# Optimization experiments

Hardware: AMD Instinct MI355X
Metric: run time of the kernel (lower is better)

Reference implementation:

```python
import jax, jax.numpy as jnp
import numpy as np

B, S, D = 1, 2048, 2048
NH, NKV = 32, 8
HD = D // NH  # 64
ROPE_THETA = 10000.0


def setup_inputs() -> dict:
    key = jax.random.key(0)
    k1, k2, k3 = jax.random.split(key, 3)
    x = jax.random.normal(k1, (B, S, D), dtype=jnp.float32)
    # real RoPE frequencies (freqs_cis = exp(i * t * theta^(-2j/hd)))
    inv_freq = 1.0 / (ROPE_THETA ** (np.arange(0, HD, 2, dtype=np.float32) / HD))
    t = np.arange(S, dtype=np.float32)
    ang = np.outer(t, inv_freq)  # [S, HD/2]
    cos = jnp.asarray(np.cos(ang), dtype=jnp.float32)
    sin = jnp.asarray(np.sin(ang), dtype=jnp.float32)
    wqkv = jax.random.normal(k2, (NH * HD + 2 * NKV * HD, D), dtype=jnp.float32) * (D ** -0.5)
    wo = jax.random.normal(k3, (D, NH * HD), dtype=jnp.float32) * (D ** -0.5)
    return {"x": x, "cos": cos, "sin": sin, "wqkv": wqkv, "wo": wo}


def _rope(t, cos, sin):
    # t: [b, h, s, hd]; pairs are interleaved (even=real, odd=imag)
    tr = t[..., 0::2]
    ti = t[..., 1::2]
    c = cos[None, None]  # [1,1,s,hd/2]
    s_ = sin[None, None]
    orr = tr * c - ti * s_
    oi = tr * s_ + ti * c
    out = jnp.stack([orr, oi], axis=-1)  # [b,h,s,hd/2,2]
    return out.reshape(t.shape)


def reference(x, cos, sin, wqkv, wo):
    bsz, seqlen, d_model = x.shape
    qkv = jnp.einsum('bsd,ed->bse', x, wqkv)  # fused QKV proj
    q, k, v = jnp.split(qkv, [NH * HD, NH * HD + NKV * HD], axis=-1)
    q = q.reshape(bsz, seqlen, NH, HD).transpose(0, 2, 1, 3)
    k = k.reshape(bsz, seqlen, NKV, HD).transpose(0, 2, 1, 3)
    v = v.reshape(bsz, seqlen, NKV, HD).transpose(0, 2, 1, 3)
    q = _rope(q, cos, sin)
    k = _rope(k, cos, sin)
    # GQA: repeat_interleave kv heads
    rep = NH // NKV
    k_r = jnp.broadcast_to(k[:, :, None], (bsz, NKV, rep, seqlen, HD)).reshape(bsz, NH, seqlen, HD)
    v_r = jnp.broadcast_to(v[:, :, None], (bsz, NKV, rep, seqlen, HD)).reshape(bsz, NH, seqlen, HD)
    scale = 1.0 / jnp.sqrt(jnp.asarray(HD, dtype=x.dtype))
    scores = jnp.einsum('bhqd,bhkd->bhqk', q, k_r) * scale
    causal = jnp.tril(jnp.ones((seqlen, seqlen), dtype=bool))
    scores = jnp.where(causal[None, None], scores, jnp.asarray(-jnp.inf, dtype=scores.dtype))
    attn = jax.nn.softmax(scores, axis=-1)
    y = jnp.einsum('bhqk,bhkd->bhqd', attn, v_r)
    y = y.transpose(0, 2, 1, 3).reshape(bsz, seqlen, NH * HD)
    y = jnp.einsum('bse,de->bsd', y, wo)
    return y
```

## Files before the change

kernel.cpp:

```cpp
#include <hip/hip_runtime.h>
#include <hip/hip_bf16.h>

typedef __attribute__((ext_vector_type(8))) short bf16x8;
typedef __attribute__((ext_vector_type(4))) float f32x4;
typedef __attribute__((ext_vector_type(16))) float f32x16;
typedef __attribute__((ext_vector_type(2))) unsigned int u32x2;

#define S_LEN 2048
#define DMODEL 2048
#define NHEAD 32
#define NKVH 8
#define HDIM 64
#define EQKV 3072

#if defined(__has_builtin)
#if __has_builtin(__builtin_amdgcn_global_load_lds)
#define HAVE_GLL 1
#endif
#endif

__device__ __forceinline__ unsigned short f2bf(float f) {
  unsigned int u = __float_as_uint(f);
  u = (u + 0x7FFFu + ((u >> 16) & 1u)) >> 16;
  return (unsigned short)u;
}

__device__ __forceinline__ f32x4 mfma16(bf16x8 a, bf16x8 b, f32x4 c) {
  return __builtin_amdgcn_mfma_f32_16x16x32_bf16(a, b, c, 0, 0, 0);
}
__device__ __forceinline__ f32x16 mfma32(bf16x8 a, bf16x8 b, f32x16 c) {
  return __builtin_amdgcn_mfma_f32_32x32x16_bf16(a, b, c, 0, 0, 0);
}

__device__ __forceinline__ unsigned cvtpk(float a, float b) {
  unsigned r;
  asm("v_cvt_pk_bf16_f32 %0, %1, %2" : "=v"(r) : "v"(a), "v"(b));
  return r;
}

__device__ __forceinline__ void plswap(unsigned& a, unsigned& b) {
  u32x2 r = __builtin_amdgcn_permlane32_swap(a, b, false, false);
  a = r.x;
  b = r.y;
}
__device__ __forceinline__ void plswapf(float& a, float& b) {
  unsigned ua = __float_as_uint(a), ub = __float_as_uint(b);
  plswap(ua, ub);
  a = __uint_as_float(ua);
  b = __uint_as_float(ub);
}

#if HAVE_GLL
__device__ __forceinline__ void gload16(const unsigned short* g,
                                        unsigned short* l) {
  __builtin_amdgcn_global_load_lds(
      (const __attribute__((address_space(1))) unsigned int*)g,
      (__attribute__((address_space(3))) unsigned int*)l, 16, 0, 0);
}
#endif

__global__ void cast_kernel(const float* __restrict__ src,
                            unsigned short* __restrict__ dst, int n4) {
  int i = blockIdx.x * blockDim.x + threadIdx.x;
  if (i >= n4) return;
  float4 v = ((const float4*)src)[i];
  ushort4 o;
  o.x = f2bf(v.x); o.y = f2bf(v.y); o.z = f2bf(v.z); o.w = f2bf(v.w);
  ((ushort4*)dst)[i] = o;
}

__launch_bounds__(256)
__global__ void gemm_bt(const unsigned short* __restrict__ A,
                        const unsigned short* __restrict__ B,
                        float* __restrict__ C, int M, int N, int K) {
  __shared__ unsigned short As[128 * 64];
  __shared__ unsigned short Bs[128 * 64];
  const int tid = threadIdx.x;
  const int w = tid >> 6, l = tid & 63;
  const int wr = w >> 1, wc = w & 1;
  const int bm = blockIdx.y, bn = blockIdx.x;
  const int lr = l & 15, lq = l >> 4;

  f32x4 acc[4][4];
#pragma unroll
  for (int m = 0; m < 4; ++m)
#pragma unroll
    for (int n = 0; n < 4; ++n) acc[m][n] = (f32x4)0.f;

  const unsigned short* gA[4];
  const unsigned short* gB[4];
#pragma unroll
  for (int i = 0; i < 4; ++i) {
    int c = i * 256 + tid;
    int row = c >> 3;
    int sc = (c & 7) ^ (row & 7);
    gA[i] = A + (size_t)(bm * 128 + row) * K + sc * 8;
    gB[i] = B + (size_t)(bn * 128 + row) * K + sc * 8;
  }

  for (int k0 = 0; k0 < K; k0 += 64) {
#if HAVE_GLL
#pragma unroll
    for (int i = 0; i < 4; ++i) {
      gload16(gA[i] + k0, &As[(i * 256 + w * 64) * 8]);
      gload16(gB[i] + k0, &Bs[(i * 256 + w * 64) * 8]);
    }
#else
#pragma unroll
    for (int i = 0; i < 4; ++i) {
      int c = i * 256 + tid;
      *(uint4*)(&As[c * 8]) = *(const uint4*)(gA[i] + k0);
      *(uint4*)(&Bs[c * 8]) = *(const uint4*)(gB[i] + k0);
    }
#endif
    __syncthreads();
#pragma unroll
    for (int ks = 0; ks < 2; ++ks) {
      bf16x8 af[4], bfr[4];
#pragma unroll
      for (int m = 0; m < 4; ++m) {
        int row = wr * 64 + m * 16 + lr;
        int ch = (ks * 4 + lq) ^ (row & 7);
        af[m] = *(const bf16x8*)(&As[row * 64 + ch * 8]);
      }
#pragma unroll
      for (int n = 0; n < 4; ++n) {
        int row = wc * 64 + n * 16 + lr;
        int ch = (ks * 4 + lq) ^ (row & 7);
        bfr[n] = *(const bf16x8*)(&Bs[row * 64 + ch * 8]);
      }
#pragma unroll
      for (int m = 0; m < 4; ++m)
#pragma unroll
        for (int n = 0; n < 4; ++n)
          acc[m][n] = mfma16(af[m], bfr[n], acc[m][n]);
    }
    __syncthreads();
  }
  const int r0 = bm * 128 + wr * 64;
  const int c0 = bn * 128 + wc * 64;
#pragma unroll
  for (int m = 0; m < 4; ++m)
#pragma unroll
    for (int n = 0; n < 4; ++n)
#pragma unroll
      for (int r = 0; r < 4; ++r)
        C[(size_t)(r0 + m * 16 + 4 * lq + r) * N + c0 + n * 16 + lr] =
            acc[m][n][r];
}

#define KSCALE 0.18033688011112042f
__global__ void rope_split(const float* __restrict__ qkv,
                           const float* __restrict__ cosb,
                           const float* __restrict__ sinb,
                           unsigned short* __restrict__ qb,
                           unsigned short* __restrict__ kft) {
  const int s = blockIdx.x;
  const float* row = qkv + (size_t)s * EQKV;
  for (int idx = threadIdx.x; idx < 1280; idx += 256) {
    int hh = idx >> 5;
    int m = idx & 31;
    float c = cosb[s * 32 + m];
    float sn = sinb[s * 32 + m];
    if (hh < 32) {
      float tr = row[hh * 64 + 2 * m];
      float ti = row[hh * 64 + 2 * m + 1];
      unsigned int pack = (unsigned int)f2bf(tr * c - ti * sn) |
                          ((unsigned int)f2bf(tr * sn + ti * c) << 16);
      *(unsigned int*)(qb + ((size_t)hh * S_LEN + s) * HDIM + 2 * m) = pack;
    } else {
      int kvh = hh - 32;
      float cs = c * KSCALE, ss = sn * KSCALE;
      float tr = row[2048 + kvh * 64 + 2 * m];
      float ti = row[2048 + kvh * 64 + 2 * m + 1];
      unsigned int pack = (unsigned int)f2bf(tr * cs - ti * ss) |
                          ((unsigned int)f2bf(tr * ss + ti * cs) << 16);
      int kt = s >> 5, lq = s & 31;
      int j = m >> 3, hi = (m >> 2) & 1;
      unsigned short* dst =
          kft +
          ((((size_t)kvh * 64 + kt) * 4 + j) * 64 + lq + 32 * hi) * 8 +
          (m & 3) * 2;
      *(unsigned int*)dst = pack;
    }
  }
}

__global__ void v_transpose(const float* __restrict__ qkv,
                            unsigned short* __restrict__ vft) {
  __shared__ unsigned short tile[64][72];
  const int kvh = blockIdx.x;
  const int st = blockIdx.y;
  const int t = threadIdx.x;
  {
    const int sl = t >> 2, dg = t & 3;
    const float* src =
        qkv + (size_t)(st * 64 + sl) * EQKV + 2560 + kvh * 64 + dg * 16;
#pragma unroll
    for (int j = 0; j < 16; ++j) tile[dg * 16 + j][sl] = f2bf(src[j]);
  }
  __syncthreads();
  {
    const int kt_local = t >> 7, c = (t >> 5) & 3, lq2 = t & 31;
    const int kt = st * 2 + kt_local;
    const int d = ((c >> 1) & 1) * 32 + lq2;
    unsigned short* dbase =
        vft + (((size_t)(kvh * 64 + kt) * 4 + c) * 64) * 8;
#pragma unroll
    for (int hi2 = 0; hi2 < 2; ++hi2) {
      int koff = kt_local * 32 + (c & 1) * 16 + 8 * hi2;
      *(uint4*)(dbase + (lq2 + 32 * hi2) * 8) =
          *(const uint4*)(&tile[d][koff]);
    }
  }
}

__launch_bounds__(256, 4)
__global__ void attn_kernel(const unsigned short* __restrict__ qb,
                            const unsigned short* __restrict__ kft,
                            const unsigned short* __restrict__ vft,
                            unsigned short* __restrict__ aob) {
  __shared__ float buf[4][64][19];
  const int tid = threadIdx.x;
  const int wv = tid >> 6, l = tid & 63;
  const int bid = blockIdx.x;
  const int h = bid & 31;
  const int qt = 63 - (bid >> 5);
  const int kvh = h >> 2;
  const int q0 = qt << 5;
  const int lq = l & 31;
  const int hi = l >> 5;
  const int qg = q0 + lq;

  const unsigned short* qrow = qb + ((size_t)h * S_LEN + qg) * HDIM + 8 * hi;
  bf16x8 qf[4];
#pragma unroll
  for (int j = 0; j < 4; ++j) qf[j] = *(const bf16x8*)(qrow + 16 * j);

  const unsigned short* kbase = kft + (size_t)kvh * 64 * 2048;
  const unsigned short* vbase = vft + (size_t)kvh * 64 * 2048;

  f32x16 o0 = (f32x16)0.f, o1 = (f32x16)0.f;
  float mrun = -1e30f, lrun = 0.f;
  const int ntile = qt + 1;

  for (int kt = wv; kt < ntile; kt += 4) {
    const int key0 = kt << 5;
    const unsigned short* kvt = kbase + (size_t)kt * 2048;
    bf16x8 kf0 = *(const bf16x8*)(kvt + l * 8);
    bf16x8 kf1 = *(const bf16x8*)(kvt + 512 + l * 8);
    bf16x8 kf2 = *(const bf16x8*)(kvt + 1024 + l * 8);
    bf16x8 kf3 = *(const bf16x8*)(kvt + 1536 + l * 8);
    const unsigned short* vvt = vbase + (size_t)kt * 2048;
    bf16x8 va00 = *(const bf16x8*)(vvt + l * 8);
    bf16x8 va01 = *(const bf16x8*)(vvt + 512 + l * 8);
    bf16x8 va10 = *(const bf16x8*)(vvt + 1024 + l * 8);
    bf16x8 va11 = *(const bf16x8*)(vvt + 1536 + l * 8);

    f32x16 s = (f32x16)0.f;
    __builtin_amdgcn_s_setprio(1);
    s = mfma32(kf0, qf[0], s);
    s = mfma32(kf1, qf[1], s);
    s = mfma32(kf2, qf[2], s);
    s = mfma32(kf3, qf[3], s);
    __builtin_amdgcn_s_setprio(0);

    float p[16];
    if (kt == ntile - 1) {
#pragma unroll
      for (int r = 0; r < 16; ++r) {
        int key = key0 + (r & 3) + 8 * (r >> 2) + 4 * hi;
        p[r] = (key > qg) ? -1e30f : s[r];
      }
    } else {
#pragma unroll
      for (int r = 0; r < 16; ++r) p[r] = s[r];
    }
    float a0 = fmaxf(fmaxf(p[0], p[1]), p[2]);
    float a1 = fmaxf(fmaxf(p[3], p[4]), p[5]);
    float a2 = fmaxf(fmaxf(p[6], p[7]), p[8]);
    float a3 = fmaxf(fmaxf(p[9], p[10]), p[11]);
    float a4 = fmaxf(fmaxf(p[12], p[13]), p[14]);
    float mt = fmaxf(fmaxf(fmaxf(a0, a1), a2), fmaxf(fmaxf(a3, a4), p[15]));
    float mto = mt;
    plswapf(mt, mto);
    mt = fmaxf(mt, mto);
    if (!__all(mt - mrun <= 8.f)) {
      float mnew = fmaxf(mrun, mt);
      float al = __builtin_amdgcn_exp2f(mrun - mnew);
      mrun = mnew;
      lrun *= al;
      o0 *= al;
      o1 *= al;
    }
#pragma unroll
    for (int r = 0; r < 16; ++r) p[r] = __builtin_amdgcn_exp2f(p[r] - mrun);
    float s0 = (p[0] + p[1]) + (p[2] + p[3]);
    float s1 = (p[4] + p[5]) + (p[6] + p[7]);
    float s2 = (p[8] + p[9]) + (p[10] + p[11]);
    float s3 = (p[12] + p[13]) + (p[14] + p[15]);
    float ts = (s0 + s1) + (s2 + s3);
    float tso = ts;
    plswapf(ts, tso);
    ts += tso;
    lrun += ts;
    union B8 { unsigned u[4]; bf16x8 v; } pb0, pb1;
    {
      unsigned t0 = cvtpk(p[0], p[1]), t1 = cvtpk(p[4], p[5]);
      plswap(t0, t1);
      pb0.u[0] = t0; pb0.u[2] = t1;
    }
    {
      unsigned t0 = cvtpk(p[2], p[3]), t1 = cvtpk(p[6], p[7]);
      plswap(t0, t1);
      pb0.u[1] = t0; pb0.u[3] = t1;
    }
    {
      unsigned t0 = cvtpk(p[8], p[9]), t1 = cvtpk(p[12], p[13]);
      plswap(t0, t1);
      pb1.u[0] = t0; pb1.u[2] = t1;
    }
    {
      unsigned t0 = cvtpk(p[10], p[11]), t1 = cvtpk(p[14], p[15]);
      plswap(t0, t1);
      pb1.u[1] = t0; pb1.u[3] = t1;
    }
    __builtin_amdgcn_s_setprio(1);
    o0 = mfma32(va00, pb0.v, o0);
    o0 = mfma32(va01, pb1.v, o0);
    o1 = mfma32(va10, pb0.v, o1);
    o1 = mfma32(va11, pb1.v, o1);
    __builtin_amdgcn_s_setprio(0);
  }

  {
    union F16 { f32x16 v; f32x4 q[4]; } uu;
    uu.v = o0;
    float* dst = &buf[wv][l][0];
#pragma unroll
    for (int i = 0; i < 4; ++i) *(f32x4*)(dst + 4 * i) = uu.q[i];
    dst[16] = mrun;
    dst[17] = lrun;
  }
  __syncthreads();
  float mfin = -1e30f;
#pragma unroll
  for (int w2 = 0; w2 < 4; ++w2) mfin = fmaxf(mfin, buf[w2][l][16]);
  float lsum = 0.f;
  float scl[4];
#pragma unroll
  for (int w2 = 0; w2 < 4; ++w2) {
    scl[w2] = __builtin_amdgcn_exp2f(buf[w2][l][16] - mfin);
    lsum += buf[w2][l][17] * scl[w2];
  }
  const float inv = 1.f / lsum;
  unsigned short* obase = aob + (size_t)qg * DMODEL + h * 64;
  {
    f32x4 acc = (f32x4)0.f;
#pragma unroll
    for (int w2 = 0; w2 < 4; ++w2)
      acc += *(const f32x4*)&buf[w2][l][wv * 4] * scl[w2];
    unsigned u0 = cvtpk(acc[0] * inv, acc[1] * inv);
    unsigned u1 = cvtpk(acc[2] * inv, acc[3] * inv);
    unsigned short* dsto = obase + 8 * wv + 4 * hi;
    *(unsigned*)(dsto) = u0;
    *(unsigned*)(dsto + 2) = u1;
  }
  __syncthreads();
  {
    union F16 { f32x16 v; f32x4 q[4]; } uu;
    uu.v = o1;
    float* dst = &buf[wv][l][0];
#pragma unroll
    for (int i = 0; i < 4; ++i) *(f32x4*)(dst + 4 * i) = uu.q[i];
  }
  __syncthreads();
  {
    f32x4 acc = (f32x4)0.f;
#pragma unroll
    for (int w2 = 0; w2 < 4; ++w2)
      acc += *(const f32x4*)&buf[w2][l][wv * 4] * scl[w2];
    unsigned u0 = cvtpk(acc[0] * inv, acc[1] * inv);
    unsigned u1 = cvtpk(acc[2] * inv, acc[3] * inv);
    unsigned short* dsto = obase + 32 + 8 * wv + 4 * hi;
    *(unsigned*)(dsto) = u0;
    *(unsigned*)(dsto + 2) = u1;
  }
}

extern "C" void kernel_launch(void* const* d_in, const int* in_sizes, int n_in,
                              void* d_out, int out_size, void* d_ws,
                              size_t ws_size, hipStream_t stream) {
  const float* x = (const float*)d_in[0];
  const float* cosb = (const float*)d_in[1];
  const float* sinb = (const float*)d_in[2];
  const float* wqkv = (const float*)d_in[3];
  const float* wo = (const float*)d_in[4];
  float* out = (float*)d_out;
  char* ws = (char*)d_ws;
  float* qkv = (float*)(ws);
  unsigned short* xb = (unsigned short*)(ws + 25165824);
  unsigned short* wb = (unsigned short*)(ws + 33554432);
  unsigned short* wob = (unsigned short*)(ws + 46137344);
  unsigned short* qb = (unsigned short*)(ws + 54525952);
  unsigned short* kft = (unsigned short*)(ws + 62914560);
  unsigned short* vft = (unsigned short*)(ws + 65011712);
  unsigned short* aob = (unsigned short*)(ws + 67108864);

  cast_kernel<<<dim3(1048576 / 256), 256, 0, stream>>>(x, xb, 1048576);
  cast_kernel<<<dim3(1572864 / 256), 256, 0, stream>>>(wqkv, wb, 1572864);
  cast_kernel<<<dim3(1048576 / 256), 256, 0, stream>>>(wo, wob, 1048576);
  gemm_bt<<<dim3(24, 16), 256, 0, stream>>>(xb, wb, qkv, 2048, 3072, 2048);
  rope_split<<<dim3(2048), 256, 0, stream>>>(qkv, cosb, sinb, qb, kft);
  v_transpose<<<dim3(8, 32), 256, 0, stream>>>(qkv, vft);
  attn_kernel<<<dim3(2048), 256, 0, stream>>>(qb, kft, vft, aob);
  gemm_bt<<<dim3(16, 16), 256, 0, stream>>>(aob, wob, out, 2048, 2048, 2048);
}
```

Before: 142.9 us.

## Double-buffer GEMM LDS tiles and swizzle workgroup order for L2 locality

The bf16 GEMM now keeps two LDS buffers per operand and issues the global-to-LDS loads for the next K tile before computing on the current one. Partial vmcnt waits and raw barriers let the loads overlap with the MFMA work. It also remaps the workgroup IDs in strides of eight to improve L2 reuse across neighbouring tiles. In exchange, LDS use doubles to 64 KB per block, which may lower occupancy, and the hand-written waitcnt values depend on the exact number of load instructions issued.

```diff
diff --git a/kernel.cpp b/kernel.cpp
--- a/kernel.cpp
+++ b/kernel.cpp
@@ -73,12 +73,15 @@
 __global__ void gemm_bt(const unsigned short* __restrict__ A,
                         const unsigned short* __restrict__ B,
                         float* __restrict__ C, int M, int N, int K) {
-  __shared__ unsigned short As[128 * 64];
-  __shared__ unsigned short Bs[128 * 64];
+  __shared__ unsigned short As[2][128 * 64];
+  __shared__ unsigned short Bs[2][128 * 64];
   const int tid = threadIdx.x;
   const int w = tid >> 6, l = tid & 63;
   const int wr = w >> 1, wc = w & 1;
-  const int bm = blockIdx.y, bn = blockIdx.x;
+  const int nwg = gridDim.x * gridDim.y;
+  const int bid0 = blockIdx.y * gridDim.x + blockIdx.x;
+  const int swz = (bid0 & 7) * (nwg >> 3) + (bid0 >> 3);
+  const int bm = swz / gridDim.x, bn = swz % gridDim.x;
   const int lr = l & 15, lq = l >> 4;
 
   f32x4 acc[4][4];
@@ -98,45 +101,75 @@
     gB[i] = B + (size_t)(bn * 128 + row) * K + sc * 8;
   }
 
-  for (int k0 = 0; k0 < K; k0 += 64) {
 #if HAVE_GLL
-#pragma unroll
-    for (int i = 0; i < 4; ++i) {
-      gload16(gA[i] + k0, &As[(i * 256 + w * 64) * 8]);
-      gload16(gB[i] + k0, &Bs[(i * 256 + w * 64) * 8]);
-    }
+#define STAGE(bufi, k0)                                        \
+  do {                                                         \
+    _Pragma("unroll") for (int i = 0; i < 4; ++i) {            \
+      gload16(gA[i] + (k0), &As[bufi][(i * 256 + w * 64) * 8]);\
+      gload16(gB[i] + (k0), &Bs[bufi][(i * 256 + w * 64) * 8]);\
+    }                                                          \
+  } while (0)
 #else
-#pragma unroll
-    for (int i = 0; i < 4; ++i) {
-      int c = i * 256 + tid;
-      *(uint4*)(&As[c * 8]) = *(const uint4*)(gA[i] + k0);
-      *(uint4*)(&Bs[c * 8]) = *(const uint4*)(gB[i] + k0);
-    }
+#define STAGE(bufi, k0)                                        \
+  do {                                                         \
+    _Pragma("unroll") for (int i = 0; i < 4; ++i) {            \
+      int c = i * 256 + tid;                                   \
+      *(uint4*)(&As[bufi][c * 8]) = *(const uint4*)(gA[i] + (k0)); \
+      *(uint4*)(&Bs[bufi][c * 8]) = *(const uint4*)(gB[i] + (k0)); \
+    }                                                          \
+  } while (0)
 #endif
+
+#define COMPUTE(bufi)                                                     \
+  do {                                                                    \
+    _Pragma("unroll") for (int ks = 0; ks < 2; ++ks) {                    \
+      bf16x8 af[4], bfr[4];                                               \
+      _Pragma("unroll") for (int m = 0; m < 4; ++m) {                     \
+        int row = wr * 64 + m * 16 + lr;                                  \
+        int ch = (ks * 4 + lq) ^ (row & 7);                               \
+        af[m] = *(const bf16x8*)(&As[bufi][row * 64 + ch * 8]);           \
+      }                                                                   \
+      _Pragma("unroll") for (int n = 0; n < 4; ++n) {                     \
+        int row = wc * 64 + n * 16 + lr;                                  \
+        int ch = (ks * 4 + lq) ^ (row & 7);                               \
+        bfr[n] = *(const bf16x8*)(&Bs[bufi][row * 64 + ch * 8]);          \
+      }                                                                   \
+      _Pragma("unroll") for (int m = 0; m < 4; ++m)                       \
+          _Pragma("unroll") for (int n = 0; n < 4; ++n)                   \
+              acc[m][n] = mfma16(af[m], bfr[n], acc[m][n]);               \
+    }                                                                     \
+  } while (0)
+
+  const int nt = K >> 6;
+  STAGE(0, 0);
+  int cur = 0;
+#if HAVE_GLL
+  for (int t = 0; t < nt - 1; ++t) {
+    STAGE(cur ^ 1, (t + 1) * 64);
+    asm volatile("s_waitcnt vmcnt(8)" ::: "memory");
+    __builtin_amdgcn_sched_barrier(0);
+    __builtin_amdgcn_s_barrier();
+    COMPUTE(cur);
+    asm volatile("s_waitcnt lgkmcnt(0)" ::: "memory");
+    __builtin_amdgcn_sched_barrier(0);
+    __builtin_amdgcn_s_barrier();
+    cur ^= 1;
+  }
+  asm volatile("s_waitcnt vmcnt(0)" ::: "memory");
+  __builtin_amdgcn_sched_barrier(0);
+  __builtin_amdgcn_s_barrier();
+  COMPUTE(cur);
+#else
+  for (int t = 0; t < nt; ++t) {
+    if (t > 0) STAGE(cur, t * 64);
     __syncthreads();
-#pragma unroll
-    for (int ks = 0; ks < 2; ++ks) {
-      bf16x8 af[4], bfr[4];
-#pragma unroll
-      for (int m = 0; m < 4; ++m) {
-        int row = wr * 64 + m * 16 + lr;
-        int ch = (ks * 4 + lq) ^ (row & 7);
-        af[m] = *(const bf16x8*)(&As[row * 64 + ch * 8]);
-      }
-#pragma unroll
-      for (int n = 0; n < 4; ++n) {
-        int row = wc * 64 + n * 16 + lr;
-        int ch = (ks * 4 + lq) ^ (row & 7);
-        bfr[n] = *(const bf16x8*)(&Bs[row * 64 + ch * 8]);
-      }
-#pragma unroll
-      for (int m = 0; m < 4; ++m)
-#pragma unroll
-        for (int n = 0; n < 4; ++n)
-          acc[m][n] = mfma16(af[m], bfr[n], acc[m][n]);
-    }
+    COMPUTE(cur);
     __syncthreads();
   }
+#endif
+#undef STAGE
+#undef COMPUTE
+
   const int r0 = bm * 128 + wr * 64;
   const int c0 = bn * 128 + wc * 64;
 #pragma unroll
```

New measurement: 134.5 us. 1.06x faster.
